# Kernel tuning notes

Hardware: AMD Instinct MI355X
Metric: run time of the kernel (lower is better)

Reference implementation:

```python
import jax, jax.numpy as jnp
from jax import lax
import numpy as np

B = 16
E, NH, FF, L = 768, 12, 3072, 8
D = E // NH  # 64, per-head dim
PATCH_DIM = 16 * 16 * 16  # 4096


def setup_inputs() -> dict:
    key = jax.random.key(0)
    ks = jax.random.split(key, 16)
    s = 0.02
    def n(k, shape):
        return jax.random.normal(k, shape, dtype=jnp.float32) * s
    return {
        "x": jax.random.normal(ks[0], (B, 512, 512, 3), dtype=jnp.float32),
        "conv1_w": n(ks[1], (3, 3, 3, 16)), "conv1_b": jnp.zeros((16,), jnp.float32),
        "conv2_w": n(ks[2], (3, 3, 16, 16)), "conv2_b": jnp.zeros((16,), jnp.float32),
        "proj_w": n(ks[3], (PATCH_DIM, E)), "proj_b": jnp.zeros((E,), jnp.float32),
        "Wq": n(ks[4], (L, E, E)), "bq": jnp.zeros((L, E), jnp.float32),
        "Wk": n(ks[5], (L, E, E)), "bk": jnp.zeros((L, E), jnp.float32),
        "Wv": n(ks[6], (L, E, E)), "bv": jnp.zeros((L, E), jnp.float32),
        "Wo": n(ks[7], (L, E, E)), "bo": jnp.zeros((L, E), jnp.float32),
        "W1": n(ks[8], (L, E, FF)), "b1": jnp.zeros((L, FF), jnp.float32),
        "W2": n(ks[9], (L, FF, E)), "b2": jnp.zeros((L, E), jnp.float32),
        "ln1_g": jnp.ones((L, E), jnp.float32), "ln1_b": jnp.zeros((L, E), jnp.float32),
        "ln2_g": jnp.ones((L, E), jnp.float32), "ln2_b": jnp.zeros((L, E), jnp.float32),
        "head_w": n(ks[10], (E, 1)), "head_b": jnp.zeros((1,), jnp.float32),
    }


def _ln(x, g, b, eps=1e-6):
    m = jnp.mean(x, axis=-1, keepdims=True)
    v = jnp.var(x, axis=-1, keepdims=True)
    return (x - m) * lax.rsqrt(v + eps) * g + b


def _forward(x, conv1_w, conv1_b, conv2_w, conv2_b, proj_w, proj_b,
             Wq, bq, Wk, bk, Wv, bv, Wo, bo, W1, b1, W2, b2,
             ln1_g, ln1_b, ln2_g, ln2_b, head_w, head_b):
    dn = ('NHWC', 'HWIO', 'NHWC')
    h = jax.nn.relu(lax.conv_general_dilated(x, conv1_w, (1, 1), 'VALID', dimension_numbers=dn) + conv1_b)
    h = lax.reduce_window(h, -jnp.inf, lax.max, (1, 2, 2, 1), (1, 2, 2, 1), 'VALID')  # (B,255,255,16)
    h = jax.nn.relu(lax.conv_general_dilated(h, conv2_w, (1, 1), 'VALID', dimension_numbers=dn) + conv2_b)
    h = lax.reduce_window(h, -jnp.inf, lax.max, (1, 2, 2, 1), (1, 2, 2, 1), 'VALID')  # (B,126,126,16)
    # tf.image.extract_patches 16x16 stride 16 SAME: pad 126 -> 128 (1 before, 1 after)
    h = jnp.pad(h, ((0, 0), (1, 1), (1, 1), (0, 0)))
    Bc = h.shape[0]
    patches = h.reshape(Bc, 8, 16, 8, 16, 16).transpose(0, 1, 3, 2, 4, 5).reshape(Bc, 64, PATCH_DIM)
    t = patches @ proj_w + proj_b  # (B,64,768)
    scale = 1.0 / jnp.sqrt(jnp.float32(D))  # tf code scales by sqrt(per-head key dim)
    for i in range(L):
        q = (t @ Wq[i] + bq[i]).reshape(Bc, -1, NH, D).transpose(0, 2, 1, 3)
        k = (t @ Wk[i] + bk[i]).reshape(Bc, -1, NH, D).transpose(0, 2, 1, 3)
        v = (t @ Wv[i] + bv[i]).reshape(Bc, -1, NH, D).transpose(0, 2, 1, 3)
        w = jax.nn.softmax(jnp.einsum('bhqd,bhkd->bhqk', q, k) * scale, axis=-1)
        a = jnp.einsum('bhqk,bhkd->bhqd', w, v)  # (B,H,S,D)
        # FAITHFUL to original: reshape (B,H,S,D) -> (B,S,E) directly (no transpose back)
        a = a.reshape(Bc, -1, E)
        a = a @ Wo[i] + bo[i]
        o1 = _ln(t + a, ln1_g[i], ln1_b[i])
        f = jax.nn.relu(o1 @ W1[i] + b1[i]) @ W2[i] + b2[i]
        t = _ln(o1 + f, ln2_g[i], ln2_b[i])
    pooled = jnp.mean(t, axis=1)  # GlobalAveragePooling1D
    return jax.nn.sigmoid(pooled @ head_w + head_b)


def reference(x, conv1_w, conv1_b, conv2_w, conv2_b, proj_w, proj_b,
              Wq, bq, Wk, bk, Wv, bv, Wo, bo, W1, b1, W2, b2,
              ln1_g, ln1_b, ln2_g, ln2_b, head_w, head_b):
    return _forward(x, conv1_w, conv1_b, conv2_w, conv2_b, proj_w, proj_b,
                    Wq, bq, Wk, bk, Wv, bv, Wo, bo, W1, b1, W2, b2,
                    ln1_g, ln1_b, ln2_g, ln2_b, head_w, head_b)
```

## Files before the change

kernel.cpp:

```cpp
#include <hip/hip_runtime.h>
#include <hip/hip_bf16.h>
#include <cstdint>
#include <cstddef>

typedef __bf16 bf16;
typedef __attribute__((ext_vector_type(8))) __bf16 bf16x8;
typedef __attribute__((ext_vector_type(4))) float f32x4;

__global__ __launch_bounds__(256) void wtrans(const float* __restrict__ src,
    bf16* __restrict__ dst, int K, int N) {
  __shared__ float tile[32][33];
  int l = blockIdx.z;
  src += (size_t)l * K * N; dst += (size_t)l * K * N;
  int n0 = blockIdx.x * 32, k0 = blockIdx.y * 32;
  int tx = threadIdx.x & 31, ty = threadIdx.x >> 5;
#pragma unroll
  for (int i = 0; i < 4; i++) {
    int k = ty + i * 8;
    tile[k][tx] = src[(size_t)(k0 + k) * N + n0 + tx];
  }
  __syncthreads();
#pragma unroll
  for (int i = 0; i < 4; i++) {
    int n = ty + i * 8;
    dst[(size_t)(n0 + n) * K + k0 + tx] = (bf16)tile[tx][n];
  }
}

__global__ __launch_bounds__(256) void conv1_mfma(const float* __restrict__ x,
    const float* __restrict__ w, const float* __restrict__ bias,
    bf16* __restrict__ out) {
  __shared__ alignas(16) bf16 xs[34 * 35 * 8];
  int t = threadIdx.x;
  int bx = blockIdx.x, by = blockIdx.y, b = blockIdx.z;
  int r0 = 32 * by, c0 = 32 * bx;
  for (int i = t; i < 34 * 35; i += 256) {
    int rr = i / 35, cc = i % 35;
    int gr = min(r0 + rr, 511), gc = min(c0 + cc, 511);
    const float* ip = x + ((size_t)(b * 512 + gr) * 512 + gc) * 3;
    bf16x8 pv = {(bf16)ip[0], (bf16)ip[1], (bf16)ip[2],
                 (bf16)0.f, (bf16)0.f, (bf16)0.f, (bf16)0.f, (bf16)0.f};
    *(bf16x8*)&xs[i * 8] = pv;
  }
  int lane = t & 63, wave = t >> 6;
  int lr = lane & 15, lq = lane >> 4;
  bf16x8 bfrag[3];
#pragma unroll
  for (int ky = 0; ky < 3; ky++) {
    bf16x8 v;
#pragma unroll
    for (int j = 0; j < 8; j++)
      v[j] = (lq < 3 && j < 3) ? (bf16)w[((ky * 3 + lq) * 3 + j) * 16 + lr] : (bf16)0.f;
    bfrag[ky] = v;
  }
  float bco = bias[lr];
  __syncthreads();
#pragma unroll
  for (int yy = 0; yy < 4; yy++) {
    int Y = wave * 4 + yy;
    int yp = by * 16 + Y;
    int cy = 2 * Y;
#pragma unroll
    for (int hx = 0; hx < 2; hx++) {
      f32x4 a0 = {0.f, 0.f, 0.f, 0.f}, a1 = {0.f, 0.f, 0.f, 0.f};
      int pbase = hx * 16 + lr + lq;
#pragma unroll
      for (int ky = 0; ky < 3; ky++) {
        bf16x8 f0 = *(const bf16x8*)&xs[((cy + ky) * 35 + pbase) * 8];
        a0 = __builtin_amdgcn_mfma_f32_16x16x32_bf16(f0, bfrag[ky], a0, 0, 0, 0);
      }
#pragma unroll
      for (int ky = 0; ky < 3; ky++) {
        bf16x8 f1 = *(const bf16x8*)&xs[((cy + 1 + ky) * 35 + pbase) * 8];
        a1 = __builtin_amdgcn_mfma_f32_16x16x32_bf16(f1, bfrag[ky], a1, 0, 0, 0);
      }
      float m0 = fmaxf(fmaxf(a0[0], a0[1]), fmaxf(a1[0], a1[1]));
      float m1 = fmaxf(fmaxf(a0[2], a0[3]), fmaxf(a1[2], a1[3]));
      m0 = fmaxf(m0 + bco, 0.f);
      m1 = fmaxf(m1 + bco, 0.f);
      int xp0 = bx * 16 + hx * 8 + 2 * lq, xp1 = xp0 + 1;
      if (yp < 255) {
        bf16* op = out + ((size_t)(b * 255 + yp) * 255) * 16 + lr;
        if (xp0 < 255) op[xp0 * 16] = (bf16)m0;
        if (xp1 < 255) op[xp1 * 16] = (bf16)m1;
      }
    }
  }
}

__global__ __launch_bounds__(256) void conv2_mfma(const bf16* __restrict__ in,
    const float* __restrict__ w, const float* __restrict__ bias,
    bf16* __restrict__ patches) {
  __shared__ alignas(16) bf16 xlo[1156 * 8];
  __shared__ alignas(16) bf16 xhi[1156 * 8];
  __shared__ float ws[2304];
  int t = threadIdx.x;
  int tx = blockIdx.x, ty = blockIdx.y, b = blockIdx.z;
  for (int i = t; i < 2304; i += 256) ws[i] = w[i];
  int r0 = 32 * ty - 2, c0 = 32 * tx - 2;
  for (int i = t; i < 1156; i += 256) {
    int rr = i / 34, cc = i % 34;
    int gr = min(max(r0 + rr, 0), 254), gc = min(max(c0 + cc, 0), 254);
    const bf16* ip = in + ((size_t)(b * 255 + gr) * 255 + gc) * 16;
    *(uint4*)&xlo[i * 8] = *(const uint4*)ip;
    *(uint4*)&xhi[i * 8] = *(const uint4*)(ip + 8);
  }
  __syncthreads();
  int lane = t & 63, wave = t >> 6;
  int lr = lane & 15, lq = lane >> 4;
  int tapsel = lq >> 1;
  int ci0 = (lq & 1) * 8;
  bf16x8 bfrag[5];
  int koff[5];
#pragma unroll
  for (int c2 = 0; c2 < 5; c2++) {
    int tap = 2 * c2 + tapsel;
    bf16x8 v;
#pragma unroll
    for (int j = 0; j < 8; j++)
      v[j] = (tap < 9) ? (bf16)ws[tap * 256 + (ci0 + j) * 16 + lr] : (bf16)0.f;
    bfrag[c2] = v;
    int tc = min(tap, 8);
    koff[c2] = (tc / 3) * 34 + (tc % 3);
  }
  const bf16* plane = (lq & 1) ? xhi : xlo;
  float bco = bias[lr];
  bf16* pout = patches + ((size_t)(b * 64 + ty * 8 + tx) * 4096);
#pragma unroll
  for (int yy = 0; yy < 4; yy++) {
    int Y = wave * 4 + yy;
    int yp = ty * 16 + Y;
    bool padrow = (yp == 0 || yp == 127);
#pragma unroll
    for (int hx = 0; hx < 2; hx++) {
      f32x4 a0 = {0.f, 0.f, 0.f, 0.f}, a1 = {0.f, 0.f, 0.f, 0.f};
      int base0 = (2 * Y) * 34 + hx * 16 + lr;
      int base1 = base0 + 34;
#pragma unroll
      for (int c2 = 0; c2 < 5; c2++) {
        bf16x8 f0 = *(const bf16x8*)&plane[(base0 + koff[c2]) * 8];
        a0 = __builtin_amdgcn_mfma_f32_16x16x32_bf16(f0, bfrag[c2], a0, 0, 0, 0);
      }
#pragma unroll
      for (int c2 = 0; c2 < 5; c2++) {
        bf16x8 f1 = *(const bf16x8*)&plane[(base1 + koff[c2]) * 8];
        a1 = __builtin_amdgcn_mfma_f32_16x16x32_bf16(f1, bfrag[c2], a1, 0, 0, 0);
      }
      float m0 = fmaxf(fmaxf(a0[0], a0[1]), fmaxf(a1[0], a1[1]));
      float m1 = fmaxf(fmaxf(a0[2], a0[3]), fmaxf(a1[2], a1[3]));
      m0 = fmaxf(m0 + bco, 0.f);
      m1 = fmaxf(m1 + bco, 0.f);
      int px0 = hx * 8 + 2 * lq, px1 = px0 + 1;
      int xp0 = tx * 16 + px0, xp1 = xp0 + 1;
      if (padrow || xp0 == 0) m0 = 0.f;
      if (padrow || xp1 == 127) m1 = 0.f;
      pout[Y * 256 + px0 * 16 + lr] = (bf16)m0;
      pout[Y * 256 + px1 * 16 + lr] = (bf16)m1;
    }
  }
}

#define LSTR 72

template<int MODE>
__device__ __forceinline__ void gemm_core(const bf16* __restrict__ A,
    const bf16* __restrict__ Bt, const float* __restrict__ bias,
    float* __restrict__ Cf, bf16* __restrict__ Cb,
    int bm, int bn, int N, int K, int k0, int kc) {
  __shared__ alignas(16) bf16 As[64 * LSTR];
  __shared__ alignas(16) bf16 Bs[64 * LSTR];
  int t = threadIdx.x, lane = t & 63, wave = t >> 6;
  int wm = (wave >> 1) * 32, wn = (wave & 1) * 32;
  int lq = lane >> 4, lr = lane & 15;
  f32x4 acc[2][2];
#pragma unroll
  for (int i = 0; i < 2; i++)
#pragma unroll
  for (int j = 0; j < 2; j++) acc[i][j] = (f32x4){0.f, 0.f, 0.f, 0.f};
  int r = t >> 2, c = (t & 3) * 16;
  const bf16* Ap = A + (size_t)(bm + r) * K + k0 + c;
  const bf16* Bp = Bt + (size_t)(bn + r) * K + k0 + c;
  bf16* AsW = &As[r * LSTR + c];
  bf16* BsW = &Bs[r * LSTR + c];
  uint4 a0 = *(const uint4*)Ap, a1 = *(const uint4*)(Ap + 8);
  uint4 b0 = *(const uint4*)Bp, b1 = *(const uint4*)(Bp + 8);
  for (int kk = 64; kk <= kc; kk += 64) {
    *(uint4*)AsW = a0; *(uint4*)(AsW + 8) = a1;
    *(uint4*)BsW = b0; *(uint4*)(BsW + 8) = b1;
    __syncthreads();
    if (kk < kc) {
      Ap += 64; Bp += 64;
      a0 = *(const uint4*)Ap; a1 = *(const uint4*)(Ap + 8);
      b0 = *(const uint4*)Bp; b1 = *(const uint4*)(Bp + 8);
    }
#pragma unroll
    for (int ks = 0; ks < 2; ks++) {
      bf16x8 af0 = *(const bf16x8*)&As[(wm + lr) * LSTR + ks * 32 + lq * 8];
      bf16x8 af1 = *(const bf16x8*)&As[(wm + 16 + lr) * LSTR + ks * 32 + lq * 8];
      bf16x8 bfr0 = *(const bf16x8*)&Bs[(wn + lr) * LSTR + ks * 32 + lq * 8];
      bf16x8 bfr1 = *(const bf16x8*)&Bs[(wn + 16 + lr) * LSTR + ks * 32 + lq * 8];
      acc[0][0] = __builtin_amdgcn_mfma_f32_16x16x32_bf16(af0, bfr0, acc[0][0], 0, 0, 0);
      acc[0][1] = __builtin_amdgcn_mfma_f32_16x16x32_bf16(af0, bfr1, acc[0][1], 0, 0, 0);
      acc[1][0] = __builtin_amdgcn_mfma_f32_16x16x32_bf16(af1, bfr0, acc[1][0], 0, 0, 0);
      acc[1][1] = __builtin_amdgcn_mfma_f32_16x16x32_bf16(af1, bfr1, acc[1][1], 0, 0, 0);
    }
    __syncthreads();
  }
#pragma unroll
  for (int mi = 0; mi < 2; mi++)
#pragma unroll
  for (int ni = 0; ni < 2; ni++) {
    int col = bn + wn + ni * 16 + lr;
#pragma unroll
    for (int rr = 0; rr < 4; rr++) {
      int row = bm + wm + mi * 16 + lq * 4 + rr;
      float v = acc[mi][ni][rr];
      if (MODE == 1) {
        v = fmaxf(v + bias[col], 0.f);
        Cb[(size_t)row * N + col] = (bf16)v;
      } else {
        Cf[(size_t)row * N + col] = v;
      }
    }
  }
}

template<int MODE>
__global__ __launch_bounds__(256) void gemm_std(const bf16* __restrict__ A,
    const bf16* __restrict__ Bt, const float* __restrict__ bias,
    float* __restrict__ Cf, bf16* __restrict__ Cb, int N, int K, int KC) {
  int s = blockIdx.z;
  float* Cfp = Cf ? Cf + (size_t)s * 1024 * N : nullptr;
  gemm_core<MODE>(A, Bt, bias, Cfp, Cb, blockIdx.y * 64, blockIdx.x * 64, N, K, s * KC, KC);
}

__global__ __launch_bounds__(256) void gemm_qkv(const bf16* __restrict__ A,
    const bf16* __restrict__ Btq, const bf16* __restrict__ Btk, const bf16* __restrict__ Btv,
    float* __restrict__ qp, float* __restrict__ kp, float* __restrict__ vp) {
  int z = blockIdx.z;
  int sel = z >> 1, s = z & 1;
  const bf16* Bt = (sel == 0) ? Btq : (sel == 1) ? Btk : Btv;
  float* C = ((sel == 0) ? qp : (sel == 1) ? kp : vp) + (size_t)s * 786432;
  gemm_core<0>(A, Bt, nullptr, C, nullptr, blockIdx.y * 64, blockIdx.x * 64, 768, 768, s * 384, 384);
}

__global__ __launch_bounds__(256) void attn_kernel(const float* __restrict__ Qp,
    const float* __restrict__ Kp, const float* __restrict__ Vp,
    const float* __restrict__ bq, const float* __restrict__ bk, const float* __restrict__ bv,
    bf16* __restrict__ Aout) {
  __shared__ alignas(16) float qs[64 * 68];
  __shared__ alignas(16) float ks[64 * 68];
  __shared__ alignas(16) float ss[64 * 68];
  int t = threadIdx.x;
  int bh = blockIdx.x; int b = bh / 12, h = bh % 12;
  size_t base = (size_t)b * 49152 + h * 64;
  const float* qb0 = Qp + base; const float* qb1 = qb0 + 786432;
  const float* kb0 = Kp + base; const float* kb1 = kb0 + 786432;
  const float* vb0 = Vp + base; const float* vb1 = vb0 + 786432;
  {
    int s = t >> 2, qd = (t & 3) * 16;
#pragma unroll
    for (int j = 0; j < 16; j += 4) {
      float4 q0 = *(const float4*)(qb0 + (size_t)s * 768 + qd + j);
      float4 q1 = *(const float4*)(qb1 + (size_t)s * 768 + qd + j);
      float4 qb4 = *(const float4*)(bq + h * 64 + qd + j);
      float4 k0 = *(const float4*)(kb0 + (size_t)s * 768 + qd + j);
      float4 k1 = *(const float4*)(kb1 + (size_t)s * 768 + qd + j);
      float4 kb4 = *(const float4*)(bk + h * 64 + qd + j);
      qs[s * 68 + qd + j + 0] = q0.x + q1.x + qb4.x;
      qs[s * 68 + qd + j + 1] = q0.y + q1.y + qb4.y;
      qs[s * 68 + qd + j + 2] = q0.z + q1.z + qb4.z;
      qs[s * 68 + qd + j + 3] = q0.w + q1.w + qb4.w;
      ks[s * 68 + qd + j + 0] = k0.x + k1.x + kb4.x;
      ks[s * 68 + qd + j + 1] = k0.y + k1.y + kb4.y;
      ks[s * 68 + qd + j + 2] = k0.z + k1.z + kb4.z;
      ks[s * 68 + qd + j + 3] = k0.w + k1.w + kb4.w;
    }
  }
  __syncthreads();
  int r = t >> 4, c = t & 15;
  {
    float sc[4][4];
#pragma unroll
    for (int i = 0; i < 4; i++)
#pragma unroll
    for (int j = 0; j < 4; j++) sc[i][j] = 0.f;
    for (int k = 0; k < 64; k += 4) {
      float4 qv[4], kv[4];
#pragma unroll
      for (int i = 0; i < 4; i++) qv[i] = *(const float4*)&qs[(r + 16 * i) * 68 + k];
#pragma unroll
      for (int j = 0; j < 4; j++) kv[j] = *(const float4*)&ks[(c + 16 * j) * 68 + k];
#pragma unroll
      for (int i = 0; i < 4; i++)
#pragma unroll
      for (int j = 0; j < 4; j++)
        sc[i][j] += qv[i].x * kv[j].x + qv[i].y * kv[j].y + qv[i].z * kv[j].z + qv[i].w * kv[j].w;
    }
#pragma unroll
    for (int i = 0; i < 4; i++)
#pragma unroll
    for (int j = 0; j < 4; j++)
      ss[(r + 16 * i) * 68 + c + 16 * j] = sc[i][j] * 0.125f;
  }
  __syncthreads();
  {
    int d = t & 63, s0 = (t >> 6) * 16;
    float bvd = bv[h * 64 + d];
    alignas(16) float vv[16];
#pragma unroll
    for (int i = 0; i < 16; i++)
      vv[i] = vb0[(size_t)(s0 + i) * 768 + d] + vb1[(size_t)(s0 + i) * 768 + d] + bvd;
#pragma unroll
    for (int i = 0; i < 16; i += 4) *(float4*)&qs[d * 68 + s0 + i] = *(float4*)&vv[i];
  }
  {
    int lane = t & 63, wave = t >> 6;
    for (int rr = 0; rr < 16; rr++) {
      int row = wave * 16 + rr;
      float v = ss[row * 68 + lane];
      float m = v;
#pragma unroll
      for (int off = 32; off > 0; off >>= 1) m = fmaxf(m, __shfl_xor(m, off));
      float e = __expf(v - m);
      float ssum = e;
#pragma unroll
      for (int off = 32; off > 0; off >>= 1) ssum += __shfl_xor(ssum, off);
      ss[row * 68 + lane] = e / ssum;
    }
  }
  __syncthreads();
  {
    float oc[4][4];
#pragma unroll
    for (int i = 0; i < 4; i++)
#pragma unroll
    for (int j = 0; j < 4; j++) oc[i][j] = 0.f;
    for (int k = 0; k < 64; k += 4) {
      float4 pv[4], vv[4];
#pragma unroll
      for (int i = 0; i < 4; i++) pv[i] = *(const float4*)&ss[(r + 16 * i) * 68 + k];
#pragma unroll
      for (int j = 0; j < 4; j++) vv[j] = *(const float4*)&qs[(c + 16 * j) * 68 + k];
#pragma unroll
      for (int i = 0; i < 4; i++)
#pragma unroll
      for (int j = 0; j < 4; j++)
        oc[i][j] += pv[i].x * vv[j].x + pv[i].y * vv[j].y + pv[i].z * vv[j].z + pv[i].w * vv[j].w;
    }
    bf16* ob = Aout + (size_t)b * 49152 + h * 4096;
#pragma unroll
    for (int i = 0; i < 4; i++)
#pragma unroll
    for (int j = 0; j < 4; j++)
      ob[(r + 16 * i) * 64 + c + 16 * j] = (bf16)oc[i][j];
  }
}

template<int S>
__global__ __launch_bounds__(256) void ln_kernel(const float* __restrict__ X,
    const float* __restrict__ Y, const float* __restrict__ yb,
    const float* __restrict__ g, const float* __restrict__ bta,
    float* __restrict__ Of, bf16* __restrict__ Ob) {
  int row = blockIdx.x, t = threadIdx.x;
  const float* xp = X + (size_t)row * 768;
  float vals[3]; float s = 0.f, s2 = 0.f;
#pragma unroll
  for (int i = 0; i < 3; i++) {
    int e = t + 256 * i;
    float v = xp[e] + yb[e];
#pragma unroll
    for (int p = 0; p < S; p++) v += Y[(size_t)p * 786432 + (size_t)row * 768 + e];
    vals[i] = v; s += v; s2 = fmaf(v, v, s2);
  }
#pragma unroll
  for (int off = 32; off > 0; off >>= 1) { s += __shfl_xor(s, off); s2 += __shfl_xor(s2, off); }
  __shared__ float rs[4], rs2[4];
  if ((t & 63) == 0) { rs[t >> 6] = s; rs2[t >> 6] = s2; }
  __syncthreads();
  s = rs[0] + rs[1] + rs[2] + rs[3];
  s2 = rs2[0] + rs2[1] + rs2[2] + rs2[3];
  float mean = s * (1.f / 768.f);
  float var = s2 * (1.f / 768.f) - mean * mean;
  float rstd = rsqrtf(var + 1e-6f);
  float* ofp = Of + (size_t)row * 768;
  bf16* obp = Ob + (size_t)row * 768;
#pragma unroll
  for (int i = 0; i < 3; i++) {
    int e = t + 256 * i;
    float o = (vals[i] - mean) * rstd * g[e] + bta[e];
    ofp[e] = o; obp[e] = (bf16)o;
  }
}

__global__ __launch_bounds__(256) void reduce2(const float* __restrict__ P,
    const float* __restrict__ bias, float* __restrict__ Of, bf16* __restrict__ Ob) {
  int row = blockIdx.x, t = threadIdx.x;
#pragma unroll
  for (int i = 0; i < 3; i++) {
    int e = t + 256 * i;
    float v = P[(size_t)row * 768 + e] + P[786432 + (size_t)row * 768 + e] + bias[e];
    Of[(size_t)row * 768 + e] = v;
    Ob[(size_t)row * 768 + e] = (bf16)v;
  }
}

__global__ __launch_bounds__(256) void head_kernel(const float* __restrict__ T,
    const float* __restrict__ hw, const float* __restrict__ hbp, float* __restrict__ out) {
  int b = blockIdx.x, t = threadIdx.x;
  float acc = 0.f;
#pragma unroll
  for (int i = 0; i < 3; i++) {
    int e = t + 256 * i;
    float s = 0.f;
    for (int si = 0; si < 64; si++) s += T[(size_t)(b * 64 + si) * 768 + e];
    acc = fmaf(s * (1.f / 64.f), hw[e], acc);
  }
#pragma unroll
  for (int off = 32; off > 0; off >>= 1) acc += __shfl_xor(acc, off);
  __shared__ float rs[4];
  if ((t & 63) == 0) rs[t >> 6] = acc;
  __syncthreads();
  if (t == 0) {
    float z = rs[0] + rs[1] + rs[2] + rs[3] + hbp[0];
    out[b] = 1.f / (1.f + expf(-z));
  }
}

extern "C" void kernel_launch(void* const* d_in, const int* in_sizes, int n_in,
                              void* d_out, int out_size, void* d_ws, size_t ws_size,
                              hipStream_t stream) {
  const float* x     = (const float*)d_in[0];
  const float* c1w   = (const float*)d_in[1];
  const float* c1b   = (const float*)d_in[2];
  const float* c2w   = (const float*)d_in[3];
  const float* c2b   = (const float*)d_in[4];
  const float* projw = (const float*)d_in[5];
  const float* projb = (const float*)d_in[6];
  const float* Wq    = (const float*)d_in[7];
  const float* bq    = (const float*)d_in[8];
  const float* Wk    = (const float*)d_in[9];
  const float* bk    = (const float*)d_in[10];
  const float* Wv    = (const float*)d_in[11];
  const float* bv    = (const float*)d_in[12];
  const float* Wo    = (const float*)d_in[13];
  const float* bo    = (const float*)d_in[14];
  const float* W1    = (const float*)d_in[15];
  const float* b1    = (const float*)d_in[16];
  const float* W2    = (const float*)d_in[17];
  const float* b2    = (const float*)d_in[18];
  const float* ln1g  = (const float*)d_in[19];
  const float* ln1b  = (const float*)d_in[20];
  const float* ln2g  = (const float*)d_in[21];
  const float* ln2b  = (const float*)d_in[22];
  const float* headw = (const float*)d_in[23];
  const float* headb = (const float*)d_in[24];
  float* out = (float*)d_out;

  char* wp = (char*)d_ws;
  auto alloc = [&](size_t bytes) { char* p = wp; wp += (bytes + 255) & ~(size_t)255; return p; };
  bf16* c1p     = (bf16*)alloc((size_t)16 * 255 * 255 * 16 * 2);
  bf16* patches = (bf16*)alloc((size_t)1024 * 4096 * 2);
  bf16* projT   = (bf16*)alloc((size_t)4096 * 768 * 2);
  bf16* WqT     = (bf16*)alloc((size_t)8 * 768 * 768 * 2);
  bf16* WkT     = (bf16*)alloc((size_t)8 * 768 * 768 * 2);
  bf16* WvT     = (bf16*)alloc((size_t)8 * 768 * 768 * 2);
  bf16* WoT     = (bf16*)alloc((size_t)8 * 768 * 768 * 2);
  bf16* W1T     = (bf16*)alloc((size_t)8 * 768 * 3072 * 2);
  bf16* W2T     = (bf16*)alloc((size_t)8 * 3072 * 768 * 2);
  float* pp     = (float*)alloc((size_t)2 * 1024 * 768 * 4);
  float* tf     = (float*)alloc((size_t)1024 * 768 * 4);
  bf16*  tb     = (bf16*)alloc((size_t)1024 * 768 * 2);
  float* qp     = (float*)alloc((size_t)2 * 1024 * 768 * 4);
  float* kp     = (float*)alloc((size_t)2 * 1024 * 768 * 4);
  float* vp     = (float*)alloc((size_t)2 * 1024 * 768 * 4);
  float* wop    = (float*)alloc((size_t)2 * 1024 * 768 * 4);
  float* w2p    = (float*)alloc((size_t)4 * 1024 * 768 * 4);
  bf16*  ab     = (bf16*)alloc((size_t)1024 * 768 * 2);
  float* o1f    = (float*)alloc((size_t)1024 * 768 * 4);
  bf16*  o1b    = (bf16*)alloc((size_t)1024 * 768 * 2);
  bf16*  hbuf   = (bf16*)alloc((size_t)1024 * 3072 * 2);

  wtrans<<<dim3(24, 128, 1), 256, 0, stream>>>(projw, projT, 4096, 768);
  wtrans<<<dim3(24, 24, 8), 256, 0, stream>>>(Wq, WqT, 768, 768);
  wtrans<<<dim3(24, 24, 8), 256, 0, stream>>>(Wk, WkT, 768, 768);
  wtrans<<<dim3(24, 24, 8), 256, 0, stream>>>(Wv, WvT, 768, 768);
  wtrans<<<dim3(24, 24, 8), 256, 0, stream>>>(Wo, WoT, 768, 768);
  wtrans<<<dim3(96, 24, 8), 256, 0, stream>>>(W1, W1T, 768, 3072);
  wtrans<<<dim3(24, 96, 8), 256, 0, stream>>>(W2, W2T, 3072, 768);

  conv1_mfma<<<dim3(16, 16, 16), 256, 0, stream>>>(x, c1w, c1b, c1p);
  conv2_mfma<<<dim3(8, 8, 16), 256, 0, stream>>>(c1p, c2w, c2b, patches);
  gemm_std<0><<<dim3(12, 16, 2), 256, 0, stream>>>(patches, projT, nullptr, pp, nullptr, 768, 4096, 2048);
  reduce2<<<1024, 256, 0, stream>>>(pp, projb, tf, tb);

  for (int i = 0; i < 8; i++) {
    gemm_qkv<<<dim3(12, 16, 6), 256, 0, stream>>>(tb,
        WqT + (size_t)i * 589824, WkT + (size_t)i * 589824, WvT + (size_t)i * 589824,
        qp, kp, vp);
    attn_kernel<<<192, 256, 0, stream>>>(qp, kp, vp,
        bq + i * 768, bk + i * 768, bv + i * 768, ab);
    gemm_std<0><<<dim3(12, 16, 2), 256, 0, stream>>>(ab, WoT + (size_t)i * 589824,
        nullptr, wop, nullptr, 768, 768, 384);
    ln_kernel<2><<<1024, 256, 0, stream>>>(tf, wop, bo + i * 768,
        ln1g + i * 768, ln1b + i * 768, o1f, o1b);
    gemm_std<1><<<dim3(48, 16, 1), 256, 0, stream>>>(o1b, W1T + (size_t)i * 2359296,
        b1 + i * 3072, nullptr, hbuf, 3072, 768, 768);
    gemm_std<0><<<dim3(12, 16, 4), 256, 0, stream>>>(hbuf, W2T + (size_t)i * 2359296,
        nullptr, w2p, nullptr, 768, 3072, 768);
    ln_kernel<4><<<1024, 256, 0, stream>>>(o1f, w2p, b2 + i * 768,
        ln2g + i * 768, ln2b + i * 768, tf, tb);
  }
  head_kernel<<<16, 256, 0, stream>>>(tf, headw, headb, out);
}
```

Before: 995.5 us.

## Replace LDS-staged GEMM with direct global-load 128x128 register-tiled MFMA

The shared GEMM core stops staging A and B tiles through LDS with barriers. Each wave now loads its MFMA fragments straight from global memory and computes a 64x64 sub-tile with 4x4 accumulators, so each block covers 128x128. All GEMM launch grids shrink to match. This removes LDS traffic and syncs and raises per-wave arithmetic intensity, but the fragment loads become strided global accesses that rely on cache, and grids get small (e.g. 96 or 192 blocks) on a chip with many CUs.

Result: slower. 1.434 ms (+44.1%).

```diff
diff --git a/kernel.cpp b/kernel.cpp
--- a/kernel.cpp
+++ b/kernel.cpp
@@ -160,60 +160,58 @@
   }
 }
 
-#define LSTR 72
-
 template<int MODE>
 __device__ __forceinline__ void gemm_core(const bf16* __restrict__ A,
     const bf16* __restrict__ Bt, const float* __restrict__ bias,
     float* __restrict__ Cf, bf16* __restrict__ Cb,
     int bm, int bn, int N, int K, int k0, int kc) {
-  __shared__ alignas(16) bf16 As[64 * LSTR];
-  __shared__ alignas(16) bf16 Bs[64 * LSTR];
-  int t = threadIdx.x, lane = t & 63, wave = t >> 6;
-  int wm = (wave >> 1) * 32, wn = (wave & 1) * 32;
+  int lane = threadIdx.x & 63, wave = threadIdx.x >> 6;
+  int wm = bm + (wave >> 1) * 64, wn = bn + (wave & 1) * 64;
   int lq = lane >> 4, lr = lane & 15;
-  f32x4 acc[2][2];
-#pragma unroll
-  for (int i = 0; i < 2; i++)
-#pragma unroll
-  for (int j = 0; j < 2; j++) acc[i][j] = (f32x4){0.f, 0.f, 0.f, 0.f};
-  int r = t >> 2, c = (t & 3) * 16;
-  const bf16* Ap = A + (size_t)(bm + r) * K + k0 + c;
-  const bf16* Bp = Bt + (size_t)(bn + r) * K + k0 + c;
-  bf16* AsW = &As[r * LSTR + c];
-  bf16* BsW = &Bs[r * LSTR + c];
-  uint4 a0 = *(const uint4*)Ap, a1 = *(const uint4*)(Ap + 8);
-  uint4 b0 = *(const uint4*)Bp, b1 = *(const uint4*)(Bp + 8);
-  for (int kk = 64; kk <= kc; kk += 64) {
-    *(uint4*)AsW = a0; *(uint4*)(AsW + 8) = a1;
-    *(uint4*)BsW = b0; *(uint4*)(BsW + 8) = b1;
-    __syncthreads();
-    if (kk < kc) {
-      Ap += 64; Bp += 64;
-      a0 = *(const uint4*)Ap; a1 = *(const uint4*)(Ap + 8);
-      b0 = *(const uint4*)Bp; b1 = *(const uint4*)(Bp + 8);
-    }
-#pragma unroll
-    for (int ks = 0; ks < 2; ks++) {
-      bf16x8 af0 = *(const bf16x8*)&As[(wm + lr) * LSTR + ks * 32 + lq * 8];
-      bf16x8 af1 = *(const bf16x8*)&As[(wm + 16 + lr) * LSTR + ks * 32 + lq * 8];
-      bf16x8 bfr0 = *(const bf16x8*)&Bs[(wn + lr) * LSTR + ks * 32 + lq * 8];
-      bf16x8 bfr1 = *(const bf16x8*)&Bs[(wn + 16 + lr) * LSTR + ks * 32 + lq * 8];
-      acc[0][0] = __builtin_amdgcn_mfma_f32_16x16x32_bf16(af0, bfr0, acc[0][0], 0, 0, 0);
-      acc[0][1] = __builtin_amdgcn_mfma_f32_16x16x32_bf16(af0, bfr1, acc[0][1], 0, 0, 0);
-      acc[1][0] = __builtin_amdgcn_mfma_f32_16x16x32_bf16(af1, bfr0, acc[1][0], 0, 0, 0);
-      acc[1][1] = __builtin_amdgcn_mfma_f32_16x16x32_bf16(af1, bfr1, acc[1][1], 0, 0, 0);
-    }
-    __syncthreads();
-  }
-#pragma unroll
-  for (int mi = 0; mi < 2; mi++)
-#pragma unroll
-  for (int ni = 0; ni < 2; ni++) {
-    int col = bn + wn + ni * 16 + lr;
+  f32x4 acc[4][4];
+#pragma unroll
+  for (int i = 0; i < 4; i++)
+#pragma unroll
+  for (int j = 0; j < 4; j++) acc[i][j] = (f32x4){0.f, 0.f, 0.f, 0.f};
+  const bf16* Ap0 = A + (size_t)(wm + lr) * K + k0 + lq * 8;
+  const bf16* Bp0 = Bt + (size_t)(wn + lr) * K + k0 + lq * 8;
+  size_t r16 = (size_t)16 * K;
+  const bf16* Ap1 = Ap0 + r16;       const bf16* Bp1 = Bp0 + r16;
+  const bf16* Ap2 = Ap1 + r16;       const bf16* Bp2 = Bp1 + r16;
+  const bf16* Ap3 = Ap2 + r16;       const bf16* Bp3 = Bp2 + r16;
+#pragma unroll 2
+  for (int kk = 0; kk < kc; kk += 32) {
+    bf16x8 af0 = *(const bf16x8*)Ap0, af1 = *(const bf16x8*)Ap1;
+    bf16x8 af2 = *(const bf16x8*)Ap2, af3 = *(const bf16x8*)Ap3;
+    bf16x8 bf0 = *(const bf16x8*)Bp0, bf1 = *(const bf16x8*)Bp1;
+    bf16x8 bf2 = *(const bf16x8*)Bp2, bf3 = *(const bf16x8*)Bp3;
+    Ap0 += 32; Ap1 += 32; Ap2 += 32; Ap3 += 32;
+    Bp0 += 32; Bp1 += 32; Bp2 += 32; Bp3 += 32;
+    acc[0][0] = __builtin_amdgcn_mfma_f32_16x16x32_bf16(af0, bf0, acc[0][0], 0, 0, 0);
+    acc[0][1] = __builtin_amdgcn_mfma_f32_16x16x32_bf16(af0, bf1, acc[0][1], 0, 0, 0);
+    acc[0][2] = __builtin_amdgcn_mfma_f32_16x16x32_bf16(af0, bf2, acc[0][2], 0, 0, 0);
+    acc[0][3] = __builtin_amdgcn_mfma_f32_16x16x32_bf16(af0, bf3, acc[0][3], 0, 0, 0);
+    acc[1][0] = __builtin_amdgcn_mfma_f32_16x16x32_bf16(af1, bf0, acc[1][0], 0, 0, 0);
+    acc[1][1] = __builtin_amdgcn_mfma_f32_16x16x32_bf16(af1, bf1, acc[1][1], 0, 0, 0);
+    acc[1][2] = __builtin_amdgcn_mfma_f32_16x16x32_bf16(af1, bf2, acc[1][2], 0, 0, 0);
+    acc[1][3] = __builtin_amdgcn_mfma_f32_16x16x32_bf16(af1, bf3, acc[1][3], 0, 0, 0);
+    acc[2][0] = __builtin_amdgcn_mfma_f32_16x16x32_bf16(af2, bf0, acc[2][0], 0, 0, 0);
+    acc[2][1] = __builtin_amdgcn_mfma_f32_16x16x32_bf16(af2, bf1, acc[2][1], 0, 0, 0);
+    acc[2][2] = __builtin_amdgcn_mfma_f32_16x16x32_bf16(af2, bf2, acc[2][2], 0, 0, 0);
+    acc[2][3] = __builtin_amdgcn_mfma_f32_16x16x32_bf16(af2, bf3, acc[2][3], 0, 0, 0);
+    acc[3][0] = __builtin_amdgcn_mfma_f32_16x16x32_bf16(af3, bf0, acc[3][0], 0, 0, 0);
+    acc[3][1] = __builtin_amdgcn_mfma_f32_16x16x32_bf16(af3, bf1, acc[3][1], 0, 0, 0);
+    acc[3][2] = __builtin_amdgcn_mfma_f32_16x16x32_bf16(af3, bf2, acc[3][2], 0, 0, 0);
+    acc[3][3] = __builtin_amdgcn_mfma_f32_16x16x32_bf16(af3, bf3, acc[3][3], 0, 0, 0);
+  }
+#pragma unroll
+  for (int mi = 0; mi < 4; mi++)
+#pragma unroll
+  for (int ni = 0; ni < 4; ni++) {
+    int col = wn + ni * 16 + lr;
 #pragma unroll
     for (int rr = 0; rr < 4; rr++) {
-      int row = bm + wm + mi * 16 + lq * 4 + rr;
+      int row = wm + mi * 16 + lq * 4 + rr;
       float v = acc[mi][ni][rr];
       if (MODE == 1) {
         v = fmaxf(v + bias[col], 0.f);
@@ -231,7 +229,7 @@
     float* __restrict__ Cf, bf16* __restrict__ Cb, int N, int K, int KC) {
   int s = blockIdx.z;
   float* Cfp = Cf ? Cf + (size_t)s * 1024 * N : nullptr;
-  gemm_core<MODE>(A, Bt, bias, Cfp, Cb, blockIdx.y * 64, blockIdx.x * 64, N, K, s * KC, KC);
+  gemm_core<MODE>(A, Bt, bias, Cfp, Cb, blockIdx.y * 128, blockIdx.x * 128, N, K, s * KC, KC);
 }
 
 __global__ __launch_bounds__(256) void gemm_qkv(const bf16* __restrict__ A,
@@ -241,7 +239,7 @@
   int sel = z >> 1, s = z & 1;
   const bf16* Bt = (sel == 0) ? Btq : (sel == 1) ? Btk : Btv;
   float* C = ((sel == 0) ? qp : (sel == 1) ? kp : vp) + (size_t)s * 786432;
-  gemm_core<0>(A, Bt, nullptr, C, nullptr, blockIdx.y * 64, blockIdx.x * 64, 768, 768, s * 384, 384);
+  gemm_core<0>(A, Bt, nullptr, C, nullptr, blockIdx.y * 128, blockIdx.x * 128, 768, 768, s * 384, 384);
 }
 
 __global__ __launch_bounds__(256) void attn_kernel(const float* __restrict__ Qp,
@@ -491,22 +489,22 @@
 
   conv1_mfma<<<dim3(16, 16, 16), 256, 0, stream>>>(x, c1w, c1b, c1p);
   conv2_mfma<<<dim3(8, 8, 16), 256, 0, stream>>>(c1p, c2w, c2b, patches);
-  gemm_std<0><<<dim3(12, 16, 2), 256, 0, stream>>>(patches, projT, nullptr, pp, nullptr, 768, 4096, 2048);
+  gemm_std<0><<<dim3(6, 8, 2), 256, 0, stream>>>(patches, projT, nullptr, pp, nullptr, 768, 4096, 2048);
   reduce2<<<1024, 256, 0, stream>>>(pp, projb, tf, tb);
 
   for (int i = 0; i < 8; i++) {
-    gemm_qkv<<<dim3(12, 16, 6), 256, 0, stream>>>(tb,
+    gemm_qkv<<<dim3(6, 8, 6), 256, 0, stream>>>(tb,
         WqT + (size_t)i * 589824, WkT + (size_t)i * 589824, WvT + (size_t)i * 589824,
         qp, kp, vp);
     attn_kernel<<<192, 256, 0, stream>>>(qp, kp, vp,
         bq + i * 768, bk + i * 768, bv + i * 768, ab);
-    gemm_std<0><<<dim3(12, 16, 2), 256, 0, stream>>>(ab, WoT + (size_t)i * 589824,
+    gemm_std<0><<<dim3(6, 8, 2), 256, 0, stream>>>(ab, WoT + (size_t)i * 589824,
         nullptr, wop, nullptr, 768, 768, 384);
     ln_kernel<2><<<1024, 256, 0, stream>>>(tf, wop, bo + i * 768,
         ln1g + i * 768, ln1b + i * 768, o1f, o1b);
-    gemm_std<1><<<dim3(48, 16, 1), 256, 0, stream>>>(o1b, W1T + (size_t)i * 2359296,
+    gemm_std<1><<<dim3(24, 8, 1), 256, 0, stream>>>(o1b, W1T + (size_t)i * 2359296,
         b1 + i * 3072, nullptr, hbuf, 3072, 768, 768);
-    gemm_std<0><<<dim3(12, 16, 4), 256, 0, stream>>>(hbuf, W2T + (size_t)i * 2359296,
+    gemm_std<0><<<dim3(6, 8, 4), 256, 0, stream>>>(hbuf, W2T + (size_t)i * 2359296,
         nullptr, w2p, nullptr, 768, 3072, 768);
     ln_kernel<4><<<1024, 256, 0, stream>>>(o1f, w2p, b2 + i * 768,
         ln2g + i * 768, ln2b + i * 768, tf, tb);
```

## Use bf16 MFMA for attention scores and PV with in-register softmax

Applied to the files above, without the earlier changes.

Rewrites the attention kernel to store Q, K, V^T and probabilities as bf16 in shared memory and compute QK^T and PV with 16x16x32 bf16 MFMA instructions instead of scalar fp32 FMAs. Softmax now runs directly on the MFMA accumulator registers using 16-lane shuffles, which removes one shared-memory round trip and a barrier. This lowers ALU and LDS cost in attention, but Q, K and the probabilities lose precision because they are rounded to bf16 before the matmuls.

Measured after the change: 910.4 us. 1.09x faster.

```diff
diff --git a/kernel.cpp b/kernel.cpp
--- a/kernel.cpp
+++ b/kernel.cpp
@@ -248,9 +248,10 @@
     const float* __restrict__ Kp, const float* __restrict__ Vp,
     const float* __restrict__ bq, const float* __restrict__ bk, const float* __restrict__ bv,
     bf16* __restrict__ Aout) {
-  __shared__ alignas(16) float qs[64 * 68];
-  __shared__ alignas(16) float ks[64 * 68];
-  __shared__ alignas(16) float ss[64 * 68];
+  __shared__ alignas(16) bf16 qs[64 * 72];
+  __shared__ alignas(16) bf16 ks[64 * 72];
+  __shared__ alignas(16) bf16 vt[64 * 72];
+  __shared__ alignas(16) bf16 ps[64 * 72];
   int t = threadIdx.x;
   int bh = blockIdx.x; int b = bh / 12, h = bh % 12;
   size_t base = (size_t)b * 49152 + h * 64;
@@ -258,103 +259,97 @@
   const float* kb0 = Kp + base; const float* kb1 = kb0 + 786432;
   const float* vb0 = Vp + base; const float* vb1 = vb0 + 786432;
   {
-    int s = t >> 2, qd = (t & 3) * 16;
+    int s = t >> 2, d0 = (t & 3) * 16;
+    alignas(16) bf16 qv[16], kv[16];
 #pragma unroll
     for (int j = 0; j < 16; j += 4) {
-      float4 q0 = *(const float4*)(qb0 + (size_t)s * 768 + qd + j);
-      float4 q1 = *(const float4*)(qb1 + (size_t)s * 768 + qd + j);
-      float4 qb4 = *(const float4*)(bq + h * 64 + qd + j);
-      float4 k0 = *(const float4*)(kb0 + (size_t)s * 768 + qd + j);
-      float4 k1 = *(const float4*)(kb1 + (size_t)s * 768 + qd + j);
-      float4 kb4 = *(const float4*)(bk + h * 64 + qd + j);
-      qs[s * 68 + qd + j + 0] = q0.x + q1.x + qb4.x;
-      qs[s * 68 + qd + j + 1] = q0.y + q1.y + qb4.y;
-      qs[s * 68 + qd + j + 2] = q0.z + q1.z + qb4.z;
-      qs[s * 68 + qd + j + 3] = q0.w + q1.w + qb4.w;
-      ks[s * 68 + qd + j + 0] = k0.x + k1.x + kb4.x;
-      ks[s * 68 + qd + j + 1] = k0.y + k1.y + kb4.y;
-      ks[s * 68 + qd + j + 2] = k0.z + k1.z + kb4.z;
-      ks[s * 68 + qd + j + 3] = k0.w + k1.w + kb4.w;
-    }
-  }
-  __syncthreads();
-  int r = t >> 4, c = t & 15;
-  {
-    float sc[4][4];
-#pragma unroll
-    for (int i = 0; i < 4; i++)
-#pragma unroll
-    for (int j = 0; j < 4; j++) sc[i][j] = 0.f;
-    for (int k = 0; k < 64; k += 4) {
-      float4 qv[4], kv[4];
-#pragma unroll
-      for (int i = 0; i < 4; i++) qv[i] = *(const float4*)&qs[(r + 16 * i) * 68 + k];
-#pragma unroll
-      for (int j = 0; j < 4; j++) kv[j] = *(const float4*)&ks[(c + 16 * j) * 68 + k];
-#pragma unroll
-      for (int i = 0; i < 4; i++)
-#pragma unroll
-      for (int j = 0; j < 4; j++)
-        sc[i][j] += qv[i].x * kv[j].x + qv[i].y * kv[j].y + qv[i].z * kv[j].z + qv[i].w * kv[j].w;
-    }
-#pragma unroll
-    for (int i = 0; i < 4; i++)
-#pragma unroll
-    for (int j = 0; j < 4; j++)
-      ss[(r + 16 * i) * 68 + c + 16 * j] = sc[i][j] * 0.125f;
-  }
-  __syncthreads();
-  {
+      float4 q0 = *(const float4*)(qb0 + (size_t)s * 768 + d0 + j);
+      float4 q1 = *(const float4*)(qb1 + (size_t)s * 768 + d0 + j);
+      float4 qb4 = *(const float4*)(bq + h * 64 + d0 + j);
+      float4 k0 = *(const float4*)(kb0 + (size_t)s * 768 + d0 + j);
+      float4 k1 = *(const float4*)(kb1 + (size_t)s * 768 + d0 + j);
+      float4 kb4 = *(const float4*)(bk + h * 64 + d0 + j);
+      qv[j + 0] = (bf16)(q0.x + q1.x + qb4.x);
+      qv[j + 1] = (bf16)(q0.y + q1.y + qb4.y);
+      qv[j + 2] = (bf16)(q0.z + q1.z + qb4.z);
+      qv[j + 3] = (bf16)(q0.w + q1.w + qb4.w);
+      kv[j + 0] = (bf16)(k0.x + k1.x + kb4.x);
+      kv[j + 1] = (bf16)(k0.y + k1.y + kb4.y);
+      kv[j + 2] = (bf16)(k0.z + k1.z + kb4.z);
+      kv[j + 3] = (bf16)(k0.w + k1.w + kb4.w);
+    }
+    *(uint4*)&qs[s * 72 + d0] = *(uint4*)&qv[0];
+    *(uint4*)&qs[s * 72 + d0 + 8] = *(uint4*)&qv[8];
+    *(uint4*)&ks[s * 72 + d0] = *(uint4*)&kv[0];
+    *(uint4*)&ks[s * 72 + d0 + 8] = *(uint4*)&kv[8];
     int d = t & 63, s0 = (t >> 6) * 16;
     float bvd = bv[h * 64 + d];
-    alignas(16) float vv[16];
+    alignas(16) bf16 vv[16];
 #pragma unroll
     for (int i = 0; i < 16; i++)
-      vv[i] = vb0[(size_t)(s0 + i) * 768 + d] + vb1[(size_t)(s0 + i) * 768 + d] + bvd;
-#pragma unroll
-    for (int i = 0; i < 16; i += 4) *(float4*)&qs[d * 68 + s0 + i] = *(float4*)&vv[i];
-  }
-  {
-    int lane = t & 63, wave = t >> 6;
-    for (int rr = 0; rr < 16; rr++) {
-      int row = wave * 16 + rr;
-      float v = ss[row * 68 + lane];
-      float m = v;
-#pragma unroll
-      for (int off = 32; off > 0; off >>= 1) m = fmaxf(m, __shfl_xor(m, off));
-      float e = __expf(v - m);
-      float ssum = e;
-#pragma unroll
-      for (int off = 32; off > 0; off >>= 1) ssum += __shfl_xor(ssum, off);
-      ss[row * 68 + lane] = e / ssum;
-    }
-  }
-  __syncthreads();
-  {
-    float oc[4][4];
-#pragma unroll
-    for (int i = 0; i < 4; i++)
-#pragma unroll
-    for (int j = 0; j < 4; j++) oc[i][j] = 0.f;
-    for (int k = 0; k < 64; k += 4) {
-      float4 pv[4], vv[4];
-#pragma unroll
-      for (int i = 0; i < 4; i++) pv[i] = *(const float4*)&ss[(r + 16 * i) * 68 + k];
-#pragma unroll
-      for (int j = 0; j < 4; j++) vv[j] = *(const float4*)&qs[(c + 16 * j) * 68 + k];
-#pragma unroll
-      for (int i = 0; i < 4; i++)
-#pragma unroll
-      for (int j = 0; j < 4; j++)
-        oc[i][j] += pv[i].x * vv[j].x + pv[i].y * vv[j].y + pv[i].z * vv[j].z + pv[i].w * vv[j].w;
-    }
-    bf16* ob = Aout + (size_t)b * 49152 + h * 4096;
-#pragma unroll
-    for (int i = 0; i < 4; i++)
-#pragma unroll
-    for (int j = 0; j < 4; j++)
-      ob[(r + 16 * i) * 64 + c + 16 * j] = (bf16)oc[i][j];
-  }
+      vv[i] = (bf16)(vb0[(size_t)(s0 + i) * 768 + d] + vb1[(size_t)(s0 + i) * 768 + d] + bvd);
+    *(uint4*)&vt[d * 72 + s0] = *(uint4*)&vv[0];
+    *(uint4*)&vt[d * 72 + s0 + 8] = *(uint4*)&vv[8];
+  }
+  __syncthreads();
+  int lane = t & 63, wave = t >> 6;
+  int lr = lane & 15, lq = lane >> 4;
+  int r0 = wave * 16;
+  f32x4 sc[4];
+#pragma unroll
+  for (int j = 0; j < 4; j++) sc[j] = (f32x4){0.f, 0.f, 0.f, 0.f};
+#pragma unroll
+  for (int kslice = 0; kslice < 2; kslice++) {
+    bf16x8 a = *(const bf16x8*)&qs[(r0 + lr) * 72 + kslice * 32 + lq * 8];
+#pragma unroll
+    for (int nj = 0; nj < 4; nj++) {
+      bf16x8 bb = *(const bf16x8*)&ks[(nj * 16 + lr) * 72 + kslice * 32 + lq * 8];
+      sc[nj] = __builtin_amdgcn_mfma_f32_16x16x32_bf16(a, bb, sc[nj], 0, 0, 0);
+    }
+  }
+#pragma unroll
+  for (int nj = 0; nj < 4; nj++)
+#pragma unroll
+  for (int rr = 0; rr < 4; rr++) sc[nj][rr] *= 0.125f;
+  float pw[4][4];
+#pragma unroll
+  for (int rr = 0; rr < 4; rr++) {
+    float m = fmaxf(fmaxf(sc[0][rr], sc[1][rr]), fmaxf(sc[2][rr], sc[3][rr]));
+#pragma unroll
+    for (int off = 1; off < 16; off <<= 1) m = fmaxf(m, __shfl_xor(m, off));
+    float e0 = __expf(sc[0][rr] - m), e1 = __expf(sc[1][rr] - m);
+    float e2 = __expf(sc[2][rr] - m), e3 = __expf(sc[3][rr] - m);
+    float sm = e0 + e1 + e2 + e3;
+#pragma unroll
+    for (int off = 1; off < 16; off <<= 1) sm += __shfl_xor(sm, off);
+    float inv = 1.f / sm;
+    pw[0][rr] = e0 * inv; pw[1][rr] = e1 * inv;
+    pw[2][rr] = e2 * inv; pw[3][rr] = e3 * inv;
+  }
+#pragma unroll
+  for (int nj = 0; nj < 4; nj++)
+#pragma unroll
+  for (int rr = 0; rr < 4; rr++)
+    ps[(r0 + lq * 4 + rr) * 72 + nj * 16 + lr] = (bf16)pw[nj][rr];
+  __syncthreads();
+  f32x4 oc[4];
+#pragma unroll
+  for (int j = 0; j < 4; j++) oc[j] = (f32x4){0.f, 0.f, 0.f, 0.f};
+#pragma unroll
+  for (int kslice = 0; kslice < 2; kslice++) {
+    bf16x8 a = *(const bf16x8*)&ps[(r0 + lr) * 72 + kslice * 32 + lq * 8];
+#pragma unroll
+    for (int nj = 0; nj < 4; nj++) {
+      bf16x8 bb = *(const bf16x8*)&vt[(nj * 16 + lr) * 72 + kslice * 32 + lq * 8];
+      oc[nj] = __builtin_amdgcn_mfma_f32_16x16x32_bf16(a, bb, oc[nj], 0, 0, 0);
+    }
+  }
+  bf16* ob = Aout + (size_t)b * 49152 + h * 4096;
+#pragma unroll
+  for (int nj = 0; nj < 4; nj++)
+#pragma unroll
+  for (int rr = 0; rr < 4; rr++)
+    ob[(r0 + lq * 4 + rr) * 64 + nj * 16 + lr] = (bf16)oc[nj][rr];
 }
 
 template<int S>
```
